# Performance work log

Measured on AMD Instinct MI355X. Metric: run time of the kernel, lower is better.

Reference implementation:

```python
import jax, jax.numpy as jnp
import numpy as np

N = 1024
R = 6
B = 64
T = 400
DECAY = 0.1
G_C = 1.0


def setup_inputs() -> dict:
    key = jax.random.key(0)
    ks = jax.random.split(key, 8)
    return {
        "hidden_0": jax.random.normal(ks[0], (N,), jnp.float32),
        "Input": jax.random.normal(ks[1], (B, T, N), jnp.float32),
        "l_Vector": jax.random.normal(ks[2], (R, N), jnp.float32),
        "r_Vector": jax.random.normal(ks[3], (R, N), jnp.float32),
        # noise_M = g_C * unscaled_noise_M; scale by 1/sqrt(N) for sane dynamics
        "noise_M": G_C * jax.random.normal(ks[4], (N, N), jnp.float32) / np.sqrt(N).astype(np.float32),
        "geom_W": jax.random.normal(ks[5], (2, N), jnp.float32) / np.sqrt(N).astype(np.float32),
        "geom_b": jax.random.normal(ks[6], (2,), jnp.float32),
        "read_W": jax.random.normal(ks[7], (6, 2), jnp.float32),
    }


def reference(hidden_0, Input, l_Vector, r_Vector, noise_M, geom_W, geom_b, read_W):
    act = jnp.tanh
    # W = r^T l / N + noise_M   -> [N, N]
    W = (r_Vector.T @ l_Vector) / N + noise_M
    h0 = jnp.broadcast_to(hidden_0, (B, N))  # hidden_0 repeated over batch

    def step(h, x_t):
        # h_{t+1} = (1-d) h + d (act(h) W^T + x_t)
        h = (1.0 - DECAY) * h + DECAY * (act(h) @ W.T + x_t)
        return h, act(h)

    # Input[:, frame, :] per step -> scan over time-major [T, B, N]
    _, hidden_t = jax.lax.scan(step, h0, jnp.swapaxes(Input, 0, 1))  # [T, B, N]

    # Note: original applies act again to hidden_t (which already holds act(hidden))
    geometry = act(hidden_t) @ geom_W.T + geom_b  # [T, B, 2]
    readout = geometry @ read_W.T  # [T, B, 6], Readout has no bias
    return hidden_t, geometry, readout
```

## Files before the change

### kernel.cpp

```cpp
#include <hip/hip_runtime.h>
#include <hip/hip_bf16.h>

#define N_DIM 1024
#define R_DIM 6
#define B_DIM 64
#define T_DIM 400
#define NBLK 128

typedef short bf16x8 __attribute__((ext_vector_type(8)));
typedef float f32x4 __attribute__((ext_vector_type(4)));

__device__ inline unsigned short f2bf(float f) {
    unsigned int u = __float_as_uint(f);
    unsigned int r = (u + 0x7fffu + ((u >> 16) & 1u)) >> 16;
    return (unsigned short)r;
}

__global__ void __launch_bounds__(64) build_wf(
    const float* __restrict__ lv,
    const float* __restrict__ rv,
    const float* __restrict__ noise,
    unsigned short* __restrict__ wf,
    unsigned* __restrict__ mbox)
{
    int blk = blockIdx.x;
    int l = threadIdx.x;
    if (blk == 0) {
#pragma unroll
        for (int k = 0; k < 64; ++k) mbox[k * 64 + l] = 0u;
    }
    int gg = blk >> 5;
    int s = blk & 31;
    int j = gg * 16 + (l & 15);
    int n0 = s * 32 + (l >> 4) * 8;
    unsigned short* dst = wf + ((size_t)blk * 64 + l) * 8;
    float rj[R_DIM];
#pragma unroll
    for (int k = 0; k < R_DIM; ++k) rj[k] = rv[k * N_DIM + j];
#pragma unroll
    for (int i = 0; i < 8; ++i) {
        int n = n0 + i;
        float acc = noise[j * N_DIM + n];
        float dot = 0.f;
#pragma unroll
        for (int k = 0; k < R_DIM; ++k) dot += rj[k] * lv[k * N_DIM + n];
        acc += dot * (1.0f / (float)N_DIM);
        dst[i] = f2bf(acc);
    }
}

__device__ __forceinline__ void publish_tile(unsigned short* dst, const float a[4],
                                             int brow0, int jcol, int l) {
    unsigned* d32 = (unsigned*)dst;
    int odd = l & 1;
    int j0 = jcol & ~1;
#pragma unroll
    for (int k = 0; k < 2; ++k) {
        float send = odd ? a[k] : a[k + 2];
        float got = __shfl_xor(send, 1);
        int row = brow0 + (odd ? (k + 2) : k);
        unsigned lo = odd ? f2bf(got)      : f2bf(a[k]);
        unsigned hi = odd ? f2bf(a[k + 2]) : f2bf(got);
        unsigned pk = lo | (hi << 16);
        unsigned* addr = d32 + ((row * N_DIM + j0) >> 1);
        asm volatile("global_store_dword %0, %1, off sc0 sc1"
                     :: "v"(addr), "v"(pk) : "memory");
    }
}

__device__ __forceinline__ void push_tag(unsigned* mbox, int w, int g, unsigned val, int l) {
    if (l < 32) {
        unsigned* addr = mbox + (w * 1024 + l * 32 + g);
        asm volatile("global_store_dword %0, %1, off sc0 sc1"
                     :: "v"(addr), "v"(val) : "memory");
    }
}

__device__ __forceinline__ void poll_mbox(const unsigned* myrow, unsigned target, int l) {
    const unsigned* p = myrow + (l & 31);
    for (;;) {
        unsigned v;
        asm volatile("global_load_dword %0, %1, off sc0 sc1\n\t"
                     "s_waitcnt vmcnt(0)"
                     : "=v"(v) : "v"(p) : "memory");
        if (__all(v >= target)) break;
        __builtin_amdgcn_s_sleep(1);
    }
}

#define LOADA(slot, off)                                                       \
    asm volatile("global_load_dwordx4 %0, %1, off offset:" #off " sc0 sc1"     \
                 : "=v"(av[slot]) : "v"(ap) : "memory");

#define LOADX(i, P)                                                            \
    asm volatile("global_load_dword %0, %1, off" : "=v"(x[i]) : "v"(P) : "memory");

#define MFMA_S(s, A0, A1)                                                      \
    A0 = __builtin_amdgcn_mfma_f32_16x16x32_bf16(av[s], wfrag[(s) * 64 + l],        A0, 0, 0, 0); \
    A1 = __builtin_amdgcn_mfma_f32_16x16x32_bf16(av[s], wfrag[(32 + (s)) * 64 + l], A1, 0, 0, 0);

__global__ void __launch_bounds__(64, 1) rnn_recurrence(
    const float* __restrict__ hidden0,
    const float* __restrict__ input,
    const unsigned short* __restrict__ wf,
    float* __restrict__ out_hidden,
    unsigned short* __restrict__ abuf0,
    unsigned short* __restrict__ abuf1,
    unsigned* __restrict__ mbox)
{
    const int w = blockIdx.x >> 5;
    const int g = blockIdx.x & 31;
    const int l = threadIdx.x;
    const int brow0 = w * 16 + (l >> 4) * 4;

    __shared__ __align__(16) unsigned short wlds[32 * 1024];
    {
        const bf16x8* src = reinterpret_cast<const bf16x8*>(wf) + (size_t)g * 4096;
        bf16x8* dstl = reinterpret_cast<bf16x8*>(wlds);
#pragma unroll
        for (int i = 0; i < 64; ++i)
            dstl[l + i * 64] = src[l + i * 64];
    }
    __syncthreads();
    const bf16x8* wfrag = reinterpret_cast<const bf16x8*>(wlds);

    int jc[2];
#pragma unroll
    for (int nt = 0; nt < 2; ++nt) jc[nt] = g * 32 + nt * 16 + (l & 15);

    float h[8];
#pragma unroll
    for (int nt = 0; nt < 2; ++nt) {
        float h0v = hidden0[jc[nt]];
#pragma unroll
        for (int i = 0; i < 4; ++i) h[nt * 4 + i] = h0v;
    }
    {
        float a0[8];
#pragma unroll
        for (int k = 0; k < 8; ++k) a0[k] = tanhf(h[k]);
#pragma unroll
        for (int nt = 0; nt < 2; ++nt)
            publish_tile(abuf0, &a0[nt * 4], brow0, jc[nt], l);
        asm volatile("s_waitcnt vmcnt(0)" ::: "memory");
        push_tag(mbox, w, g, 1u, l);
    }

    const int aoff_us = (w * 16 + (l & 15)) * N_DIM + (l >> 4) * 8;
    const unsigned* myrow = mbox + (w * 1024 + g * 32);

    for (int t = 0; t < T_DIM; ++t) {
        const unsigned short* acur = (t & 1) ? abuf1 : abuf0;
        unsigned short* anext = (t & 1) ? abuf0 : abuf1;
        const unsigned short* ap = acur + aoff_us;

        poll_mbox(myrow, (unsigned)(t + 1), l);

        bf16x8 av[32];
        LOADA(0, 0)     LOADA(1, 64)    LOADA(2, 128)   LOADA(3, 192)
        LOADA(4, 256)   LOADA(5, 320)   LOADA(6, 384)   LOADA(7, 448)
        LOADA(8, 512)   LOADA(9, 576)   LOADA(10, 640)  LOADA(11, 704)
        LOADA(12, 768)  LOADA(13, 832)  LOADA(14, 896)  LOADA(15, 960)
        LOADA(16, 1024) LOADA(17, 1088) LOADA(18, 1152) LOADA(19, 1216)
        LOADA(20, 1280) LOADA(21, 1344) LOADA(22, 1408) LOADA(23, 1472)
        LOADA(24, 1536) LOADA(25, 1600) LOADA(26, 1664) LOADA(27, 1728)
        LOADA(28, 1792) LOADA(29, 1856) LOADA(30, 1920) LOADA(31, 1984)

        float x[8];
#pragma unroll
        for (int nt = 0; nt < 2; ++nt)
#pragma unroll
            for (int i = 0; i < 4; ++i) {
                const float* xp = input + ((size_t)(brow0 + i) * T_DIM + t) * N_DIM + jc[nt];
                LOADX(nt * 4 + i, xp)
            }

        f32x4 a0e = {0.f, 0.f, 0.f, 0.f};
        f32x4 a0o = {0.f, 0.f, 0.f, 0.f};
        f32x4 a1e = {0.f, 0.f, 0.f, 0.f};
        f32x4 a1o = {0.f, 0.f, 0.f, 0.f};

        asm volatile("s_waitcnt vmcnt(32)" ::: "memory");
        __builtin_amdgcn_sched_barrier(0);
        MFMA_S(0, a0e, a1e) MFMA_S(1, a0o, a1o) MFMA_S(2, a0e, a1e) MFMA_S(3, a0o, a1o)
        MFMA_S(4, a0e, a1e) MFMA_S(5, a0o, a1o) MFMA_S(6, a0e, a1e) MFMA_S(7, a0o, a1o)
        asm volatile("s_waitcnt vmcnt(24)" ::: "memory");
        __builtin_amdgcn_sched_barrier(0);
        MFMA_S(8, a0e, a1e)  MFMA_S(9, a0o, a1o)  MFMA_S(10, a0e, a1e) MFMA_S(11, a0o, a1o)
        MFMA_S(12, a0e, a1e) MFMA_S(13, a0o, a1o) MFMA_S(14, a0e, a1e) MFMA_S(15, a0o, a1o)
        asm volatile("s_waitcnt vmcnt(16)" ::: "memory");
        __builtin_amdgcn_sched_barrier(0);
        MFMA_S(16, a0e, a1e) MFMA_S(17, a0o, a1o) MFMA_S(18, a0e, a1e) MFMA_S(19, a0o, a1o)
        MFMA_S(20, a0e, a1e) MFMA_S(21, a0o, a1o) MFMA_S(22, a0e, a1e) MFMA_S(23, a0o, a1o)
        asm volatile("s_waitcnt vmcnt(8)" ::: "memory");
        __builtin_amdgcn_sched_barrier(0);
        MFMA_S(24, a0e, a1e) MFMA_S(25, a0o, a1o) MFMA_S(26, a0e, a1e) MFMA_S(27, a0o, a1o)
        MFMA_S(28, a0e, a1e) MFMA_S(29, a0o, a1o) MFMA_S(30, a0e, a1e) MFMA_S(31, a0o, a1o)

        asm volatile("s_waitcnt vmcnt(0)" ::: "memory");
        __builtin_amdgcn_sched_barrier(0);

        f32x4 acc0 = a0e + a0o;
        f32x4 acc1 = a1e + a1o;

        float a[8];
#pragma unroll
        for (int i = 0; i < 4; ++i) {
            float hn;
            hn = 0.9f * h[0 + i] + 0.1f * (acc0[i] + x[0 + i]); h[0 + i] = hn; a[0 + i] = tanhf(hn);
            hn = 0.9f * h[4 + i] + 0.1f * (acc1[i] + x[4 + i]); h[4 + i] = hn; a[4 + i] = tanhf(hn);
        }

        if (t + 1 < T_DIM) {
#pragma unroll
            for (int nt = 0; nt < 2; ++nt)
                publish_tile(anext, &a[nt * 4], brow0, jc[nt], l);
            asm volatile("s_waitcnt vmcnt(0)" ::: "memory");
            push_tag(mbox, w, g, (unsigned)(t + 2), l);
        }
#pragma unroll
        for (int nt = 0; nt < 2; ++nt)
#pragma unroll
            for (int i = 0; i < 4; ++i)
                out_hidden[((size_t)t * B_DIM + (brow0 + i)) * N_DIM + jc[nt]] = a[nt * 4 + i];
    }
}

__global__ void __launch_bounds__(256) geo_kernel(
    const float* __restrict__ hid,
    const float* __restrict__ gW,
    const float* __restrict__ gb,
    const float* __restrict__ rW,
    float* __restrict__ geo,
    float* __restrict__ ro)
{
    int row = blockIdx.x * 4 + (threadIdx.x >> 6);
    int l = threadIdx.x & 63;
    const float* hrow = hid + (size_t)row * N_DIM;
    float a0 = 0.f, a1 = 0.f;
#pragma unroll
    for (int i = 0; i < N_DIM / 64; ++i) {
        int idx = i * 64 + l;
        float th = tanhf(hrow[idx]);
        a0 += th * gW[idx];
        a1 += th * gW[N_DIM + idx];
    }
#pragma unroll
    for (int off = 32; off; off >>= 1) {
        a0 += __shfl_down(a0, off);
        a1 += __shfl_down(a1, off);
    }
    if (l == 0) {
        float g0 = a0 + gb[0];
        float g1 = a1 + gb[1];
        geo[(size_t)row * 2 + 0] = g0;
        geo[(size_t)row * 2 + 1] = g1;
#pragma unroll
        for (int m = 0; m < 6; ++m)
            ro[(size_t)row * 6 + m] = g0 * rW[m * 2] + g1 * rW[m * 2 + 1];
    }
}

extern "C" void kernel_launch(void* const* d_in, const int* in_sizes, int n_in,
                              void* d_out, int out_size, void* d_ws, size_t ws_size,
                              hipStream_t stream) {
    const float* hidden0 = (const float*)d_in[0];
    const float* input   = (const float*)d_in[1];
    const float* lv      = (const float*)d_in[2];
    const float* rv      = (const float*)d_in[3];
    const float* noise   = (const float*)d_in[4];
    const float* gW      = (const float*)d_in[5];
    const float* gb      = (const float*)d_in[6];
    const float* rW      = (const float*)d_in[7];

    float* out_hidden = (float*)d_out;
    float* geo = out_hidden + (size_t)T_DIM * B_DIM * N_DIM;
    float* ro  = geo + (size_t)T_DIM * B_DIM * 2;

    unsigned short* wf    = (unsigned short*)d_ws;
    unsigned short* abuf0 = wf + (size_t)64 * 32 * 64 * 8;
    unsigned short* abuf1 = abuf0 + (size_t)B_DIM * N_DIM;
    unsigned* mbox = (unsigned*)(abuf1 + (size_t)B_DIM * N_DIM);

    build_wf<<<2048, 64, 0, stream>>>(lv, rv, noise, wf, mbox);

    void* args[] = { (void*)&hidden0, (void*)&input, (void*)&wf,
                     (void*)&out_hidden, (void*)&abuf0, (void*)&abuf1, (void*)&mbox };
    hipError_t e = hipLaunchCooperativeKernel((const void*)rnn_recurrence,
                                              dim3(NBLK), dim3(64), args, 0, stream);
    if (e != hipSuccess) {
        rnn_recurrence<<<dim3(NBLK), dim3(64), 0, stream>>>(
            hidden0, input, wf, out_hidden, abuf0, abuf1, mbox);
    }

    geo_kernel<<<(T_DIM * B_DIM) / 4, 256, 0, stream>>>(out_hidden, gW, gb, rW, geo, ro);
}
```

Before: 1.509 ms.

## Prefetch next-step input, pipeline mailbox polling, use fast tanh in recurrence

```diff
diff --git a/kernel.cpp b/kernel.cpp
--- a/kernel.cpp
+++ b/kernel.cpp
@@ -14,6 +14,11 @@
     unsigned int u = __float_as_uint(f);
     unsigned int r = (u + 0x7fffu + ((u >> 16) & 1u)) >> 16;
     return (unsigned short)r;
+}
+
+__device__ __forceinline__ float ftanh(float v) {
+    float e = __expf(2.0f * v);
+    return (e - 1.0f) * __builtin_amdgcn_rcpf(e + 1.0f);
 }
 
 __global__ void __launch_bounds__(64) build_wf(
@@ -76,24 +81,14 @@
     }
 }
 
-__device__ __forceinline__ void poll_mbox(const unsigned* myrow, unsigned target, int l) {
-    const unsigned* p = myrow + (l & 31);
-    for (;;) {
-        unsigned v;
-        asm volatile("global_load_dword %0, %1, off sc0 sc1\n\t"
-                     "s_waitcnt vmcnt(0)"
-                     : "=v"(v) : "v"(p) : "memory");
-        if (__all(v >= target)) break;
-        __builtin_amdgcn_s_sleep(1);
-    }
-}
-
 #define LOADA(slot, off)                                                       \
     asm volatile("global_load_dwordx4 %0, %1, off offset:" #off " sc0 sc1"     \
                  : "=v"(av[slot]) : "v"(ap) : "memory");
-
 #define LOADX(i, P)                                                            \
-    asm volatile("global_load_dword %0, %1, off" : "=v"(x[i]) : "v"(P) : "memory");
+    asm volatile("global_load_dword %0, %1, off" : "=v"(xn[i]) : "v"(P) : "memory");
+#define LOADP(dst, P)                                                          \
+    asm volatile("global_load_dword %0, %1, off sc0 sc1"                       \
+                 : "=v"(dst) : "v"(P) : "memory");
 
 #define MFMA_S(s, A0, A1)                                                      \
     A0 = __builtin_amdgcn_mfma_f32_16x16x32_bf16(av[s], wfrag[(s) * 64 + l],        A0, 0, 0, 0); \
@@ -135,26 +130,48 @@
 #pragma unroll
         for (int i = 0; i < 4; ++i) h[nt * 4 + i] = h0v;
     }
+    float x[8], xn[8];
+#pragma unroll
+    for (int nt = 0; nt < 2; ++nt)
+#pragma unroll
+        for (int i = 0; i < 4; ++i) {
+            const float* xp = input + ((size_t)(brow0 + i) * T_DIM + 0) * N_DIM + jc[nt];
+            LOADX(nt * 4 + i, xp)
+        }
     {
         float a0[8];
 #pragma unroll
-        for (int k = 0; k < 8; ++k) a0[k] = tanhf(h[k]);
+        for (int k = 0; k < 8; ++k) a0[k] = ftanh(h[k]);
 #pragma unroll
         for (int nt = 0; nt < 2; ++nt)
             publish_tile(abuf0, &a0[nt * 4], brow0, jc[nt], l);
         asm volatile("s_waitcnt vmcnt(0)" ::: "memory");
+#pragma unroll
+        for (int k = 0; k < 8; ++k) x[k] = xn[k];
         push_tag(mbox, w, g, 1u, l);
     }
 
     const int aoff_us = (w * 16 + (l & 15)) * N_DIM + (l >> 4) * 8;
     const unsigned* myrow = mbox + (w * 1024 + g * 32);
+    const unsigned* pollp = myrow + (l & 31);
 
     for (int t = 0; t < T_DIM; ++t) {
         const unsigned short* acur = (t & 1) ? abuf1 : abuf0;
         unsigned short* anext = (t & 1) ? abuf0 : abuf1;
         const unsigned short* ap = acur + aoff_us;
-
-        poll_mbox(myrow, (unsigned)(t + 1), l);
+        const unsigned target = (unsigned)(t + 1);
+
+        unsigned pv0, pv1;
+        LOADP(pv0, pollp)
+        for (;;) {
+            LOADP(pv1, pollp)
+            asm volatile("s_waitcnt vmcnt(1)" ::: "memory");
+            if (__all(pv0 >= target)) break;
+            LOADP(pv0, pollp)
+            asm volatile("s_waitcnt vmcnt(1)" ::: "memory");
+            if (__all(pv1 >= target)) break;
+            __builtin_amdgcn_s_sleep(1);
+        }
 
         bf16x8 av[32];
         LOADA(0, 0)     LOADA(1, 64)    LOADA(2, 128)   LOADA(3, 192)
@@ -166,12 +183,12 @@
         LOADA(24, 1536) LOADA(25, 1600) LOADA(26, 1664) LOADA(27, 1728)
         LOADA(28, 1792) LOADA(29, 1856) LOADA(30, 1920) LOADA(31, 1984)
 
-        float x[8];
+        int tn = (t + 1 < T_DIM) ? (t + 1) : t;
 #pragma unroll
         for (int nt = 0; nt < 2; ++nt)
 #pragma unroll
             for (int i = 0; i < 4; ++i) {
-                const float* xp = input + ((size_t)(brow0 + i) * T_DIM + t) * N_DIM + jc[nt];
+                const float* xp = input + ((size_t)(brow0 + i) * T_DIM + tn) * N_DIM + jc[nt];
                 LOADX(nt * 4 + i, xp)
             }
 
@@ -197,9 +214,6 @@
         MFMA_S(24, a0e, a1e) MFMA_S(25, a0o, a1o) MFMA_S(26, a0e, a1e) MFMA_S(27, a0o, a1o)
         MFMA_S(28, a0e, a1e) MFMA_S(29, a0o, a1o) MFMA_S(30, a0e, a1e) MFMA_S(31, a0o, a1o)
 
-        asm volatile("s_waitcnt vmcnt(0)" ::: "memory");
-        __builtin_amdgcn_sched_barrier(0);
-
         f32x4 acc0 = a0e + a0o;
         f32x4 acc1 = a1e + a1o;
 
@@ -207,22 +221,28 @@
 #pragma unroll
         for (int i = 0; i < 4; ++i) {
             float hn;
-            hn = 0.9f * h[0 + i] + 0.1f * (acc0[i] + x[0 + i]); h[0 + i] = hn; a[0 + i] = tanhf(hn);
-            hn = 0.9f * h[4 + i] + 0.1f * (acc1[i] + x[4 + i]); h[4 + i] = hn; a[4 + i] = tanhf(hn);
+            hn = 0.9f * h[0 + i] + 0.1f * (acc0[i] + x[0 + i]); h[0 + i] = hn; a[0 + i] = ftanh(hn);
+            hn = 0.9f * h[4 + i] + 0.1f * (acc1[i] + x[4 + i]); h[4 + i] = hn; a[4 + i] = ftanh(hn);
         }
 
         if (t + 1 < T_DIM) {
 #pragma unroll
             for (int nt = 0; nt < 2; ++nt)
                 publish_tile(anext, &a[nt * 4], brow0, jc[nt], l);
-            asm volatile("s_waitcnt vmcnt(0)" ::: "memory");
-            push_tag(mbox, w, g, (unsigned)(t + 2), l);
         }
 #pragma unroll
         for (int nt = 0; nt < 2; ++nt)
 #pragma unroll
             for (int i = 0; i < 4; ++i)
                 out_hidden[((size_t)t * B_DIM + (brow0 + i)) * N_DIM + jc[nt]] = a[nt * 4 + i];
+
+        asm volatile("s_waitcnt vmcnt(0)" ::: "memory");
+        asm volatile("" :: "v"(pv0), "v"(pv1));
+#pragma unroll
+        for (int k = 0; k < 8; ++k) x[k] = xn[k];
+
+        if (t + 1 < T_DIM)
+            push_tag(mbox, w, g, (unsigned)(t + 2), l);
     }
 }
 
```

New measurement: 1.325 ms. 1.14x faster.
